# Performance work log

Hardware: AMD Instinct MI355X
Metric: run time of the kernel (lower is better)

The kernel has to match this reference:

```python
import jax, jax.numpy as jnp
import numpy as np

V_MIN = -10.0
V_MAX = 10.0
NUM_ATOMS = 51
ATOM_DELTA = (V_MAX - V_MIN) / (NUM_ATOMS - 1)
BS = 1_000_000


def setup_inputs() -> dict:
    key = jax.random.key(0)
    k1, k2 = jax.random.split(key)
    reward = jax.random.normal(k1, (BS,), dtype=jnp.float32) * 3.0
    probs = jax.random.uniform(k2, (BS, NUM_ATOMS), dtype=jnp.float32)
    atom_values = (V_MIN + ATOM_DELTA * jnp.arange(NUM_ATOMS)).astype(jnp.float32)
    return {"reward": reward, "probs": probs, "atom_values": atom_values}


def reference(reward, probs, atom_values):
    # Categorical (C51) Bellman projection, expressed as a scatter-add
    # instead of the original's dense [bs, A, A] projection matrix + bmm.
    bs, A = probs.shape
    # shifted & clamped atom support: [bs, A]
    new_vals = jnp.clip(atom_values[None, :] + reward[:, None], V_MIN, V_MAX)
    idx = (new_vals - V_MIN) / ATOM_DELTA           # fractional atom index
    lower = jnp.floor(idx)
    upper = jnp.ceil(idx)
    same = lower == upper                           # idx landed exactly on an atom
    l_coef = jnp.where(same, 1.0, upper - idx)      # original sets 1.0 when l == u
    u_coef = idx - lower                            # 0 when same
    li = lower.astype(jnp.int32)
    ui = upper.astype(jnp.int32)
    rows = jnp.broadcast_to(jnp.arange(bs)[:, None], (bs, A))
    out = jnp.zeros_like(probs)
    out = out.at[rows, li].add(l_coef * probs)
    out = out.at[rows, ui].add(u_coef * probs)
    return out
```

## Files before the change

kernel.cpp:

```cpp
#include <hip/hip_runtime.h>

#define NA 51
#define ROWS 64
#define GUARD 56
#define NDATA (ROWS * NA)
#define KCLAMP 52

__global__ __launch_bounds__(ROWS, 3) void c51_bellman_kernel(
    const float* __restrict__ reward,
    const float* __restrict__ probs,
    float* __restrict__ out,
    int bs)
{
    __shared__ float lds[GUARD + NDATA + GUARD];
    float* data = lds + GUARD;
    const int tid   = threadIdx.x;
    const int row0  = blockIdx.x * ROWS;
    const int nrows = min(ROWS, bs - row0);

    float s = 0.0f;
    if (tid < nrows) s = reward[row0 + tid] * 2.5f;

    if (nrows == ROWS) {
        const char* src = (const char*)(probs + (size_t)row0 * NA);
        #pragma unroll
        for (int t = 0; t < 12; ++t) {
            __builtin_amdgcn_global_load_lds(
                (const __attribute__((address_space(1))) void*)
                    (unsigned long long)(src + t * 1024 + tid * 16),
                (__attribute__((address_space(3))) void*)
                    (unsigned long long)(data + t * 256),
                16, 0, 0);
        }
        if (tid < 48) {
            const float4 v = *(const float4*)(src + 12288 + (size_t)tid * 16);
            *(float4*)(data + 3072 + tid * 4) = v;
        }
    } else {
        const int nelem = nrows * NA;
        for (int e = tid; e < nelem; e += ROWS)
            data[e] = probs[(size_t)row0 * NA + e];
    }
    asm volatile("s_waitcnt vmcnt(0) lgkmcnt(0)" ::: "memory");
    __builtin_amdgcn_sched_barrier(0);

    if (tid < nrows) {
        const float kf = floorf(s);
        const float f  = s - kf;
        int k = (int)kf;
        k = min(max(k, -KCLAMP), KCLAMP);

        const float* rp = data + tid * NA;

        float m_lo = 0.0f, m_hi = 0.0f;
        #pragma unroll
        for (int j = 0; j < NA; ++j) {
            const float pj = rp[j];
            const float t  = (float)j + s;
            if (t < 0.0f)  m_lo += pj;
            if (t > 50.0f) m_hi += pj;
        }

        const float* wb = data + tid * NA - k - 1;
        float w[52];
        #pragma unroll
        for (int m = 0; m < 52; ++m) w[m] = wb[m];

        float* wp = data + tid * NA;
        const float w1 = 1.0f - f;
        float prev = ((unsigned)(-k - 1) <= 50u) ? w[0] : 0.0f;
        #pragma unroll
        for (int i = 0; i < NA; ++i) {
            const float cur = ((unsigned)(i - k) <= 50u) ? w[i + 1] : 0.0f;
            float o;
            if (i == 0)           o = w1 * cur + m_lo;
            else if (i == NA - 1) o = ((f == 0.0f) ? cur : f * prev) + m_hi;
            else                  o = w1 * cur + f * prev;
            wp[i] = o;
            prev = cur;
        }
    }
    asm volatile("s_waitcnt lgkmcnt(0)" ::: "memory");
    __builtin_amdgcn_sched_barrier(0);

    if (nrows == ROWS) {
        float4* o4 = (float4*)(out + (size_t)row0 * NA);
        const float4* l4 = (const float4*)data;
        #pragma unroll
        for (int t = 0; t < 12; ++t) o4[t * 64 + tid] = l4[t * 64 + tid];
        if (tid < 48) o4[768 + tid] = l4[768 + tid];
    } else {
        const int nelem = nrows * NA;
        for (int e = tid; e < nelem; e += ROWS)
            out[(size_t)row0 * NA + e] = data[e];
    }
}

extern "C" void kernel_launch(void* const* d_in, const int* in_sizes, int n_in,
                              void* d_out, int out_size, void* d_ws, size_t ws_size,
                              hipStream_t stream) {
    const float* reward = (const float*)d_in[0];
    const float* probs  = (const float*)d_in[1];
    float* out = (float*)d_out;
    const int bs = in_sizes[0];

    const int blocks = (bs + ROWS - 1) / ROWS;
    c51_bellman_kernel<<<blocks, ROWS, 0, stream>>>(reward, probs, out, bs);
}
```

Baseline: 344.7 us.

## Persistent grid with double-buffered LDS tile prefetch and nontemporal stores

Replaces the one-tile-per-block launch with a persistent grid of up to 1536 blocks. Each block walks tiles with a grid stride and double-buffers them in LDS, so the async global-to-LDS load of the next tile overlaps compute and store of the current one. Output stores become nontemporal, and the tail rows are handled directly from global memory by block 0. The cost is double the LDS per block and a lower occupancy hint, which limits latency hiding to the explicit prefetch. The vmcnt(14) wait also assumes that exactly 13 vector-memory ops are issued per tile.

```diff
diff --git a/kernel.cpp b/kernel.cpp
--- a/kernel.cpp
+++ b/kernel.cpp
@@ -4,52 +4,57 @@
 #define ROWS 64
 #define GUARD 56
 #define NDATA (ROWS * NA)
+#define BUFSZ (GUARD + NDATA + GUARD)
 #define KCLAMP 52
+#define NBLK 1536
 
-__global__ __launch_bounds__(ROWS, 3) void c51_bellman_kernel(
+typedef float v4 __attribute__((ext_vector_type(4), aligned(16)));
+
+#define WAITV(N) do { asm volatile("s_waitcnt vmcnt(" #N ")" ::: "memory"); \
+                      __builtin_amdgcn_sched_barrier(0); } while (0)
+
+__global__ __launch_bounds__(ROWS, 2) void c51_bellman_kernel(
     const float* __restrict__ reward,
     const float* __restrict__ probs,
     float* __restrict__ out,
     int bs)
 {
-    __shared__ float lds[GUARD + NDATA + GUARD];
-    float* data = lds + GUARD;
+    __shared__ __align__(16) float bufA[BUFSZ];
+    __shared__ __align__(16) float bufB[BUFSZ];
+    float* const dA = bufA + GUARD;
+    float* const dB = bufB + GUARD;
     const int tid   = threadIdx.x;
-    const int row0  = blockIdx.x * ROWS;
-    const int nrows = min(ROWS, bs - row0);
+    const int gs    = gridDim.x;
+    const int nfull = bs / ROWS;
+    const int rem   = bs - nfull * ROWS;
 
-    float s = 0.0f;
-    if (tid < nrows) s = reward[row0 + tid] * 2.5f;
-
-    if (nrows == ROWS) {
-        const char* src = (const char*)(probs + (size_t)row0 * NA);
+    auto issueL = [&](long tile, float* dst) {
+        const char* src = (const char*)probs + (size_t)tile * (NDATA * 4);
         #pragma unroll
-        for (int t = 0; t < 12; ++t) {
+        for (int c = 0; c < 12; ++c) {
             __builtin_amdgcn_global_load_lds(
                 (const __attribute__((address_space(1))) void*)
-                    (unsigned long long)(src + t * 1024 + tid * 16),
+                    (unsigned long long)(src + c * 1024 + tid * 16),
                 (__attribute__((address_space(3))) void*)
-                    (unsigned long long)(data + t * 256),
+                    (unsigned long long)(dst + c * 256),
                 16, 0, 0);
         }
         if (tid < 48) {
-            const float4 v = *(const float4*)(src + 12288 + (size_t)tid * 16);
-            *(float4*)(data + 3072 + tid * 4) = v;
+            __builtin_amdgcn_global_load_lds(
+                (const __attribute__((address_space(1))) void*)
+                    (unsigned long long)(src + 12288 + tid * 16),
+                (__attribute__((address_space(3))) void*)
+                    (unsigned long long)(dst + 3072),
+                16, 0, 0);
         }
-    } else {
-        const int nelem = nrows * NA;
-        for (int e = tid; e < nelem; e += ROWS)
-            data[e] = probs[(size_t)row0 * NA + e];
-    }
-    asm volatile("s_waitcnt vmcnt(0) lgkmcnt(0)" ::: "memory");
-    __builtin_amdgcn_sched_barrier(0);
+    };
 
-    if (tid < nrows) {
+    auto computeT = [&](float* data, float rw) {
+        const float s  = rw * 2.5f;
         const float kf = floorf(s);
         const float f  = s - kf;
         int k = (int)kf;
         k = min(max(k, -KCLAMP), KCLAMP);
-
         const float* rp = data + tid * NA;
 
         float m_lo = 0.0f, m_hi = 0.0f;
@@ -61,7 +66,7 @@
             if (t > 50.0f) m_hi += pj;
         }
 
-        const float* wb = data + tid * NA - k - 1;
+        const float* wb = rp - k - 1;
         float w[52];
         #pragma unroll
         for (int m = 0; m < 52; ++m) w[m] = wb[m];
@@ -79,20 +84,79 @@
             wp[i] = o;
             prev = cur;
         }
+    };
+
+    auto storeT = [&](const float* data, long tile) {
+        const v4* l4 = (const v4*)data;
+        v4* o4 = (v4*)(out + (size_t)tile * NDATA);
+        #pragma unroll
+        for (int m = 0; m < 12; ++m)
+            __builtin_nontemporal_store(l4[m * 64 + tid], o4 + m * 64 + tid);
+        if (tid < 48)
+            __builtin_nontemporal_store(l4[768 + tid], o4 + 768 + tid);
+    };
+
+    long t = blockIdx.x;
+    if (t < nfull) {
+        float rwA = reward[t * ROWS + tid];
+        issueL(t, dA);
+        for (;;) {
+            const long tB = t + gs;
+            const bool hB = tB < nfull;
+            float rwB = 0.0f;
+            if (hB) { rwB = reward[tB * ROWS + tid]; issueL(tB, dB); WAITV(14); }
+            else    { WAITV(0); }
+            computeT(dA, rwA);
+            storeT(dA, t);
+            if (!hB) break;
+
+            const long tA2 = tB + gs;
+            const bool hA = tA2 < nfull;
+            if (hA) { rwA = reward[tA2 * ROWS + tid]; issueL(tA2, dA); WAITV(14); }
+            else    { WAITV(0); }
+            computeT(dB, rwB);
+            storeT(dB, tB);
+            if (!hA) break;
+            t = tA2;
+        }
     }
-    asm volatile("s_waitcnt lgkmcnt(0)" ::: "memory");
-    __builtin_amdgcn_sched_barrier(0);
 
-    if (nrows == ROWS) {
-        float4* o4 = (float4*)(out + (size_t)row0 * NA);
-        const float4* l4 = (const float4*)data;
-        #pragma unroll
-        for (int t = 0; t < 12; ++t) o4[t * 64 + tid] = l4[t * 64 + tid];
-        if (tid < 48) o4[768 + tid] = l4[768 + tid];
-    } else {
-        const int nelem = nrows * NA;
-        for (int e = tid; e < nelem; e += ROWS)
-            out[(size_t)row0 * NA + e] = data[e];
+    if (rem && blockIdx.x == 0) {
+        const int r = nfull * ROWS + tid;
+        if (r < bs) {
+            const float s  = reward[r] * 2.5f;
+            const float kf = floorf(s);
+            const float f  = s - kf;
+            int k = (int)kf; k = min(max(k, -KCLAMP), KCLAMP);
+            const float* rp = probs + (size_t)r * NA;
+            float row[NA];
+            #pragma unroll
+            for (int j = 0; j < NA; ++j) row[j] = rp[j];
+            float m_lo = 0.0f, m_hi = 0.0f;
+            #pragma unroll
+            for (int j = 0; j < NA; ++j) {
+                const float tt = (float)j + s;
+                if (tt < 0.0f)  m_lo += row[j];
+                if (tt > 50.0f) m_hi += row[j];
+            }
+            float w[52];
+            #pragma unroll
+            for (int m = 0; m < 52; ++m)
+                w[m] = row[min(max(m - k - 1, 0), NA - 1)];
+            float* op = out + (size_t)r * NA;
+            const float w1 = 1.0f - f;
+            float prev = ((unsigned)(-k - 1) <= 50u) ? w[0] : 0.0f;
+            #pragma unroll
+            for (int i = 0; i < NA; ++i) {
+                const float cur = ((unsigned)(i - k) <= 50u) ? w[i + 1] : 0.0f;
+                float o;
+                if (i == 0)           o = w1 * cur + m_lo;
+                else if (i == NA - 1) o = ((f == 0.0f) ? cur : f * prev) + m_hi;
+                else                  o = w1 * cur + f * prev;
+                op[i] = o;
+                prev = cur;
+            }
+        }
     }
 }
 
@@ -104,6 +168,8 @@
     float* out = (float*)d_out;
     const int bs = in_sizes[0];
 
-    const int blocks = (bs + ROWS - 1) / ROWS;
+    const int nfull = bs / ROWS;
+    int blocks = nfull < NBLK ? nfull : NBLK;
+    if (blocks < 1) blocks = 1;
     c51_bellman_kernel<<<blocks, ROWS, 0, stream>>>(reward, probs, out, bs);
 }
```

Result: slower. 389.4 us (+13.0%).
